# Optimization experiments

Hardware: AMD Instinct MI355X
Metric: run time of the kernel (lower is better)

## Reference

```python
import jax, jax.numpy as jnp
import numpy as np

N = 10000      # nodes
E = 160000     # edges (before self-loops)
H = 8          # heads
D_IN, D_H1, D_H2 = 165, 128, 1    # per-head channels of gat1 / gat2
HID = H * D_H1                    # 1024


def batchnorm(x, gamma, beta, eps=1e-5):
    # training-mode BatchNorm1d: biased batch statistics over the node axis
    mu = x.mean(0)
    var = x.var(0)
    return (x - mu) * jax.lax.rsqrt(var + eps) * gamma + beta


def gatv2(x, src, dst, Wl, bl, Wr, br, att, bias, heads, out_ch, concat, n_nodes):
    # PyG GATv2Conv: lin_l on source, lin_r on target; e = att . LeakyReLU(xl_j + xr_i)
    xl = (x @ Wl + bl).reshape(n_nodes, heads, out_ch)   # source transform
    xr = (x @ Wr + br).reshape(n_nodes, heads, out_ch)   # target transform
    e = jax.nn.leaky_relu(xl[src] + xr[dst], 0.2)        # [E,H,C]
    logits = jnp.einsum('ehc,hc->eh', e, att)            # [E,H]
    # segment softmax over incoming edges of each destination node
    m = jax.lax.stop_gradient(jax.ops.segment_max(logits, dst, num_segments=n_nodes))
    a = jnp.exp(logits - m[dst])
    s = jax.ops.segment_sum(a, dst, num_segments=n_nodes)
    alpha = a / (s[dst] + 1e-16)                          # [E,H]
    out = jax.ops.segment_sum(xl[src] * alpha[..., None], dst, num_segments=n_nodes)
    out = out.reshape(n_nodes, heads * out_ch) if concat else out.mean(1)
    return out + bias


def setup_inputs() -> dict:
    key = jax.random.key(0)
    ks = jax.random.split(key, 12)
    g = lambda k, shape, fan_in: jax.random.normal(k, shape, jnp.float32) * (1.0 / np.sqrt(fan_in))
    return {
        'x': jax.random.normal(ks[0], (N, D_IN), jnp.float32),
        'gamma1': jnp.ones((D_IN,), jnp.float32),
        'beta1': jnp.zeros((D_IN,), jnp.float32),
        'Wl1': g(ks[1], (D_IN, HID), D_IN),
        'bl1': jnp.zeros((HID,), jnp.float32),
        'Wr1': g(ks[2], (D_IN, HID), D_IN),
        'br1': jnp.zeros((HID,), jnp.float32),
        'att1': g(ks[3], (H, D_H1), D_H1),
        'bias1': jnp.zeros((HID,), jnp.float32),
        'gamma2': jnp.ones((HID,), jnp.float32),
        'beta2': jnp.zeros((HID,), jnp.float32),
        'Wl2': g(ks[4], (HID, H * D_H2), HID),
        'bl2': jnp.zeros((H * D_H2,), jnp.float32),
        'Wr2': g(ks[5], (HID, H * D_H2), HID),
        'br2': jnp.zeros((H * D_H2,), jnp.float32),
        'att2': g(ks[6], (H, D_H2), D_H2),
        'bias2': jnp.zeros((D_H2,), jnp.float32),
        'edge_index': jax.random.randint(ks[7], (2, E), 0, N, jnp.int64 if jax.config.jax_enable_x64 else jnp.int32),
    }


def reference(x, gamma1, beta1, Wl1, bl1, Wr1, br1, att1, bias1,
              gamma2, beta2, Wl2, bl2, Wr2, br2, att2, bias2, edge_index):
    loops = jnp.arange(N, dtype=edge_index.dtype)
    src = jnp.concatenate([edge_index[0], loops])   # add_self_loops=True (PyG default)
    dst = jnp.concatenate([edge_index[1], loops])
    h = batchnorm(x, gamma1, beta1)
    h = gatv2(h, src, dst, Wl1, bl1, Wr1, br1, att1, bias1, H, D_H1, True, N)
    h = batchnorm(h, gamma2, beta2)
    h = jax.nn.leaky_relu(h, 0.01)                  # F.leaky_relu default slope
    out = gatv2(h, src, dst, Wl2, bl2, Wr2, br2, att2, bias2, H, D_H2, False, N)
    return out
```

## Files before the change

### kernel.cpp

```cpp
#include <hip/hip_runtime.h>

#define NN   10000
#define E0   160000
#define ET   170000
#define DIN  165
#define KP   192
#define HID  1024
#define NH   8
#define BP   200
#define K2P  1032


typedef __bf16 bf16x8 __attribute__((ext_vector_type(8)));
typedef float  f32x4  __attribute__((ext_vector_type(4)));

__device__ __forceinline__ float bf2f(unsigned short u) {
    unsigned int i = ((unsigned int)u) << 16;
    return __builtin_bit_cast(float, i);
}
__device__ __forceinline__ unsigned short f2bf(float f) {
    unsigned int i = __builtin_bit_cast(unsigned int, f);
    i += 0x7fffu + ((i >> 16) & 1u);
    return (unsigned short)(i >> 16);
}
__device__ __forceinline__ float fin(float x) {
    return fminf(fmaxf(x, -1e30f), 1e30f);
}
__device__ __forceinline__ int clampi(int s) {
    return min(max(s, 0), NN - 1);
}
__device__ __forceinline__ void unpack8(uint4 u, float* f) {
    f[0]=bf2f((unsigned short)(u.x)); f[1]=bf2f((unsigned short)(u.x>>16));
    f[2]=bf2f((unsigned short)(u.y)); f[3]=bf2f((unsigned short)(u.y>>16));
    f[4]=bf2f((unsigned short)(u.z)); f[5]=bf2f((unsigned short)(u.z>>16));
    f[6]=bf2f((unsigned short)(u.w)); f[7]=bf2f((unsigned short)(u.w>>16));
}

__global__ __launch_bounds__(256) void debug_fill(float* __restrict__ out, float val) {
    int i = blockIdx.x * 256 + threadIdx.x;
    if (i < NN) out[i] = val;
}

__global__ __launch_bounds__(256) void bn1_stats(const float* __restrict__ x,
                                                 float* __restrict__ colsum, float* __restrict__ colsq) {
    int r0 = blockIdx.x * 125;
    int c = threadIdx.x;
    if (c >= DIN) return;
    float acc = 0.f, sq = 0.f;
    for (int r = r0; r < r0 + 125; ++r) {
        float v = x[(size_t)r * DIN + c];
        acc += v; sq += v * v;
    }
    atomicAdd(&colsum[c], acc);
    atomicAdd(&colsq[c], sq);
}

__global__ __launch_bounds__(256) void bn1_apply(const float* __restrict__ x,
                                                 const float* __restrict__ colsum, const float* __restrict__ colsq,
                                                 const float* __restrict__ gamma, const float* __restrict__ beta,
                                                 unsigned short* __restrict__ hn) {
    int idx = blockIdx.x * 256 + threadIdx.x;
    if (idx >= NN * KP) return;
    int r = idx / KP, c = idx - r * KP;
    float v = 0.f;
    if (c < DIN) {
        float mu  = colsum[c] * (1.f / NN);
        float var = fmaxf(colsq[c] * (1.f / NN) - mu * mu, 0.f);
        float a = gamma[c] * rsqrtf(var + 1e-5f);
        float b = beta[c] - mu * a;
        v = fin(x[(size_t)r * DIN + c] * a + b);
    }
    hn[idx] = f2bf(v);
}

__global__ __launch_bounds__(256) void w1_transpose(const float* __restrict__ wl,
                                                    const float* __restrict__ wr,
                                                    unsigned short* __restrict__ wlt,
                                                    unsigned short* __restrict__ wrt) {
    const float* src    = blockIdx.z ? wr  : wl;
    unsigned short* dst = blockIdx.z ? wrt : wlt;
    __shared__ float ts[32][65];
    const int k0 = blockIdx.x * 32;
    const int n0 = blockIdx.y * 64;
    const int tid = threadIdx.x;
    for (int idx = tid; idx < 32 * 64; idx += 256) {
        int k = idx >> 6, n = idx & 63;
        ts[k][n] = (k0 + k < DIN) ? src[(size_t)(k0 + k) * HID + n0 + n] : 0.f;
    }
    __syncthreads();
    for (int idx = tid; idx < 64 * 32; idx += 256) {
        int n = idx >> 5, k = idx & 31;
        dst[(size_t)(n0 + n) * KP + k0 + k] = f2bf(ts[k][n]);
    }
}

__global__ __launch_bounds__(256) void gemm1_kernel(
    const unsigned short* __restrict__ hn,
    const unsigned short* __restrict__ wlt,
    const unsigned short* __restrict__ wrt,
    const float* __restrict__ bl,
    const float* __restrict__ br,
    unsigned short* __restrict__ xl,
    unsigned short* __restrict__ xr) {
    __shared__ unsigned short bs[2][64 * BP];
    const int tid  = threadIdx.x;
    const int lane = tid & 63;
    const int wave = tid >> 6;
    const int col  = lane & 15;
    const int q    = lane >> 4;
    const int n0   = blockIdx.y * 64;

    for (int idx = tid; idx < 64 * 48 * 2; idx += 256) {
        int z = idx >= 64 * 48;
        int rem = z ? idx - 64 * 48 : idx;
        int r = rem / 48, c = rem - r * 48;
        const unsigned short* wt = z ? wrt : wlt;
        uint2 v = *(const uint2*)(wt + (size_t)(n0 + r) * KP + c * 4);
        *(uint2*)&bs[z][r * BP + c * 4] = v;
    }
    __syncthreads();

    const int mbase = blockIdx.x * 128 + wave * 32;
    const int am0 = mbase + col;
    const int am1 = am0 + 16;
    const bool aok0 = (am0 < NN), aok1 = (am1 < NN);

    f32x4 accL[2][4], accR[2][4];
    #pragma unroll
    for (int m = 0; m < 2; ++m)
        for (int nt = 0; nt < 4; ++nt)
            for (int r = 0; r < 4; ++r) { accL[m][nt][r] = 0.f; accR[m][nt][r] = 0.f; }

    #pragma unroll
    for (int kt = 0; kt < 6; ++kt) {
        const int kk = kt * 32 + q * 8;
        uint4 a0u = make_uint4(0u,0u,0u,0u), a1u = make_uint4(0u,0u,0u,0u);
        if (aok0) a0u = *(const uint4*)(hn + (size_t)am0 * KP + kk);
        if (aok1) a1u = *(const uint4*)(hn + (size_t)am1 * KP + kk);
        bf16x8 a0 = __builtin_bit_cast(bf16x8, a0u);
        bf16x8 a1 = __builtin_bit_cast(bf16x8, a1u);
        #pragma unroll
        for (int nt = 0; nt < 4; ++nt) {
            bf16x8 bfl = __builtin_bit_cast(bf16x8, *(const uint4*)&bs[0][(nt * 16 + col) * BP + kk]);
            accL[0][nt] = __builtin_amdgcn_mfma_f32_16x16x32_bf16(a0, bfl, accL[0][nt], 0, 0, 0);
            accL[1][nt] = __builtin_amdgcn_mfma_f32_16x16x32_bf16(a1, bfl, accL[1][nt], 0, 0, 0);
            bf16x8 bfr = __builtin_bit_cast(bf16x8, *(const uint4*)&bs[1][(nt * 16 + col) * BP + kk]);
            accR[0][nt] = __builtin_amdgcn_mfma_f32_16x16x32_bf16(a0, bfr, accR[0][nt], 0, 0, 0);
            accR[1][nt] = __builtin_amdgcn_mfma_f32_16x16x32_bf16(a1, bfr, accR[1][nt], 0, 0, 0);
        }
    }

    #pragma unroll
    for (int nt = 0; nt < 4; ++nt) {
        const int nc = n0 + nt * 16 + col;
        const float bLv = bl[nc];
        const float bRv = br[nc];
        #pragma unroll
        for (int m = 0; m < 2; ++m) {
            #pragma unroll
            for (int r = 0; r < 4; ++r) {
                const int row = mbase + m * 16 + q * 4 + r;
                if (row < NN) {
                    xl[(size_t)row * HID + nc] = f2bf(fin(accL[m][nt][r] + bLv));
                    xr[(size_t)row * HID + nc] = f2bf(fin(accR[m][nt][r] + bRv));
                }
            }
        }
    }
}

__global__ __launch_bounds__(256) void edge_hist(const int* __restrict__ ei, int* __restrict__ deg) {
    int e = blockIdx.x * 256 + threadIdx.x;
    if (e >= ET) return;
    int d = (e < E0) ? ei[E0 + e] : (e - E0);
    atomicAdd(&deg[clampi(d)], 1);
}

__global__ __launch_bounds__(1024) void scan_kernel(const int* __restrict__ deg,
                                                    int* __restrict__ offs, int* __restrict__ cur,
                                                    int* __restrict__ perm) {
    __shared__ int wsum[16];
    __shared__ int bins[64];
    __shared__ int bcur[64];
    const int tid = threadIdx.x;
    const int base = tid * 10;
    int loc[10];
    int run = 0;
    #pragma unroll
    for (int j = 0; j < 10; ++j) {
        int idx = base + j;
        int v = (idx < NN) ? deg[idx] : 0;
        loc[j] = run;
        run += v;
    }
    const int lane = tid & 63;
    const int w = tid >> 6;
    int inc = run;
    #pragma unroll
    for (int s = 1; s < 64; s <<= 1) {
        int t = __shfl_up(inc, s);
        if (lane >= s) inc += t;
    }
    if (lane == 63) wsum[w] = inc;
    if (tid < 64) bins[tid] = 0;
    __syncthreads();
    int woff = 0;
    #pragma unroll
    for (int k = 0; k < 16; ++k) woff += (k < w) ? wsum[k] : 0;
    const int toff = woff + inc - run;
    #pragma unroll
    for (int j = 0; j < 10; ++j) {
        int idx = base + j;
        if (idx < NN) {
            int e = toff + loc[j]; offs[idx] = e; cur[idx] = e;
            atomicAdd(&bins[63 - min(deg[idx], 63)], 1);
        }
    }
    if (tid == 1023) offs[NN] = woff + inc;
    __syncthreads();
    if (tid < 64) {
        int v = bins[tid];
        int binc = v;
        #pragma unroll
        for (int s = 1; s < 64; s <<= 1) {
            int t = __shfl_up(binc, s);
            if (tid >= s) binc += t;
        }
        bcur[tid] = binc - v;
    }
    __syncthreads();
    #pragma unroll
    for (int j = 0; j < 10; ++j) {
        int idx = base + j;
        if (idx < NN) {
            int pos = atomicAdd(&bcur[63 - min(deg[idx], 63)], 1);
            perm[pos] = idx;
        }
    }
}

__global__ __launch_bounds__(256) void edge_scatter(const int* __restrict__ ei,
                                                    int* __restrict__ cur, int* __restrict__ ssrc) {
    int e = blockIdx.x * 256 + threadIdx.x;
    if (e >= ET) return;
    int s, d;
    if (e < E0) { s = ei[e]; d = ei[E0 + e]; }
    else        { s = e - E0; d = e - E0; }
    int pos = atomicAdd(&cur[clampi(d)], 1);
    if (pos >= 0 && pos < ET) ssrc[pos] = clampi(s);
}

__global__ __launch_bounds__(256) void gat1_node(
    const unsigned short* __restrict__ xl1, const unsigned short* xr1,
    const float* __restrict__ att1, const float* __restrict__ bias1,
    const int* __restrict__ offs, const int* __restrict__ ssrc,
    const int* __restrict__ perm,
    unsigned short* agg) {
    const int lane = threadIdx.x & 63;
    const int wave = threadIdx.x >> 6;
    const int i = perm[blockIdx.x * 4 + wave];
    const int e0 = offs[i];
    const int e1 = max(offs[i + 1], e0);

    float xr_r[16], att_r[16];
    {
        const uint4* xp = (const uint4*)(xr1 + (size_t)i * HID + lane * 16);
        uint4 u0 = xp[0], u1 = xp[1];
        unpack8(u0, xr_r); unpack8(u1, xr_r + 8);
        const float4* ap = (const float4*)(att1 + lane * 16);
        float4 a0 = ap[0], a1 = ap[1], a2 = ap[2], a3 = ap[3];
        att_r[0]=a0.x; att_r[1]=a0.y; att_r[2]=a0.z; att_r[3]=a0.w;
        att_r[4]=a1.x; att_r[5]=a1.y; att_r[6]=a1.z; att_r[7]=a1.w;
        att_r[8]=a2.x; att_r[9]=a2.y; att_r[10]=a2.z; att_r[11]=a2.w;
        att_r[12]=a3.x; att_r[13]=a3.y; att_r[14]=a3.z; att_r[15]=a3.w;
    }

    float o[16];
    #pragma unroll
    for (int j = 0; j < 16; ++j) o[j] = 0.f;
    float s = 0.f;

    int e = e0;
    for (; e + 1 < e1; e += 2) {
        const int s0i = clampi(ssrc[e]);
        const int s1i = clampi(ssrc[e + 1]);
        const uint4* xp0 = (const uint4*)(xl1 + (size_t)s0i * HID + lane * 16);
        const uint4* xp1 = (const uint4*)(xl1 + (size_t)s1i * HID + lane * 16);
        uint4 a0 = xp0[0], a1 = xp0[1], b0 = xp1[0], b1 = xp1[1];
        float xv0[16], xv1[16];
        unpack8(a0, xv0); unpack8(a1, xv0 + 8);
        unpack8(b0, xv1); unpack8(b1, xv1 + 8);
        float p0 = 0.f, p1 = 0.f;
        #pragma unroll
        for (int j = 0; j < 16; ++j) {
            float v0 = xv0[j] + xr_r[j];
            float v1 = xv1[j] + xr_r[j];
            v0 = fmaxf(v0, 0.2f * v0);
            v1 = fmaxf(v1, 0.2f * v1);
            p0 = fmaf(att_r[j], v0, p0);
            p1 = fmaf(att_r[j], v1, p1);
        }
        p0 += __shfl_xor(p0, 1); p0 += __shfl_xor(p0, 2); p0 += __shfl_xor(p0, 4);
        p1 += __shfl_xor(p1, 1); p1 += __shfl_xor(p1, 2); p1 += __shfl_xor(p1, 4);
        const float aa0 = __expf(fminf(fin(p0), 50.f));
        const float aa1 = __expf(fminf(fin(p1), 50.f));
        s += aa0 + aa1;
        #pragma unroll
        for (int j = 0; j < 16; ++j) o[j] = fmaf(aa0, xv0[j], fmaf(aa1, xv1[j], o[j]));
    }
    if (e < e1) {
        const int sidx = clampi(ssrc[e]);
        const uint4* xp = (const uint4*)(xl1 + (size_t)sidx * HID + lane * 16);
        uint4 u0 = xp[0], u1 = xp[1];
        float xv[16];
        unpack8(u0, xv); unpack8(u1, xv + 8);
        float p = 0.f;
        #pragma unroll
        for (int j = 0; j < 16; ++j) {
            float v = xv[j] + xr_r[j];
            v = fmaxf(v, 0.2f * v);
            p = fmaf(att_r[j], v, p);
        }
        p += __shfl_xor(p, 1); p += __shfl_xor(p, 2); p += __shfl_xor(p, 4);
        const float a = __expf(fminf(fin(p), 50.f));
        s += a;
        #pragma unroll
        for (int j = 0; j < 16; ++j) o[j] = fmaf(a, xv[j], o[j]);
    }

    const float inv = 1.f / (s + 1e-16f);
    const float4* bp = (const float4*)(bias1 + lane * 16);
    float4 b0 = bp[0], b1 = bp[1], b2 = bp[2], b3 = bp[3];
    float bb[16] = {b0.x,b0.y,b0.z,b0.w, b1.x,b1.y,b1.z,b1.w,
                    b2.x,b2.y,b2.z,b2.w, b3.x,b3.y,b3.z,b3.w};
    unsigned short ov[16];
    #pragma unroll
    for (int j = 0; j < 16; ++j) ov[j] = f2bf(fin(o[j] * inv + bb[j]));
    uint4* op = (uint4*)(agg + (size_t)i * HID + lane * 16);
    op[0] = *(const uint4*)&ov[0];
    op[1] = *(const uint4*)&ov[8];
}

__global__ __launch_bounds__(256) void bn2_stats(const unsigned short* __restrict__ agg,
                                                 float* __restrict__ colsum, float* __restrict__ colsq) {
    int r0 = blockIdx.x * 125;
    int t = threadIdx.x;
    float s0=0,s1=0,s2=0,s3=0,q0=0,q1=0,q2=0,q3=0;
    for (int r = r0; r < r0 + 125; ++r) {
        const ushort4 u = *(const ushort4*)(agg + (size_t)r * HID + t * 4);
        float v0=bf2f(u.x), v1=bf2f(u.y), v2=bf2f(u.z), v3=bf2f(u.w);
        s0+=v0; q0+=v0*v0; s1+=v1; q1+=v1*v1;
        s2+=v2; q2+=v2*v2; s3+=v3; q3+=v3*v3;
    }
    atomicAdd(&colsum[t*4+0], s0); atomicAdd(&colsq[t*4+0], q0);
    atomicAdd(&colsum[t*4+1], s1); atomicAdd(&colsq[t*4+1], q1);
    atomicAdd(&colsum[t*4+2], s2); atomicAdd(&colsq[t*4+2], q2);
    atomicAdd(&colsum[t*4+3], s3); atomicAdd(&colsq[t*4+3], q3);
}

__global__ __launch_bounds__(256) void gemm2_kernel(
    const unsigned short* __restrict__ agg,
    const float* __restrict__ colsum, const float* __restrict__ colsq,
    const float* __restrict__ gamma, const float* __restrict__ beta,
    const float* __restrict__ wl2, const float* __restrict__ wr2,
    const float* __restrict__ bl2, const float* __restrict__ br2,
    float* __restrict__ xl2, float* __restrict__ xr2) {
    __shared__ unsigned short bs[16 * K2P];
    __shared__ float a2s[HID], b2s[HID];
    const int tid  = threadIdx.x;
    const int lane = tid & 63;
    const int wave = tid >> 6;
    const int col  = lane & 15;
    const int q    = lane >> 4;

    for (int idx = tid; idx < 16 * HID; idx += 256) {
        int n = idx >> 10, k = idx & (HID - 1);
        float v = (n < 8) ? wl2[k * 8 + n] : wr2[k * 8 + (n - 8)];
        bs[n * K2P + k] = f2bf(v);
    }
    for (int c = tid; c < HID; c += 256) {
        float mu  = colsum[c] * (1.f / NN);
        float var = fmaxf(colsq[c] * (1.f / NN) - mu * mu, 0.f);
        float a = gamma[c] * rsqrtf(var + 1e-5f);
        a2s[c] = a; b2s[c] = beta[c] - mu * a;
    }
    __syncthreads();

    const int mtile = blockIdx.x * 4 + wave;
    if (mtile >= NN / 16) return;
    const int m0 = mtile * 16;
    const int am = m0 + col;

    f32x4 acc;
    acc[0] = acc[1] = acc[2] = acc[3] = 0.f;
    #pragma unroll
    for (int kt = 0; kt < 32; ++kt) {
        const int kk = kt * 32 + q * 8;
        uint4 u = *(const uint4*)(agg + (size_t)am * HID + kk);
        float xv[8];
        unpack8(u, xv);
        unsigned short hv[8];
        #pragma unroll
        for (int j = 0; j < 8; ++j) {
            float v = xv[j] * a2s[kk + j] + b2s[kk + j];
            v = fmaxf(v, 0.01f * v);
            hv[j] = f2bf(fin(v));
        }
        bf16x8 af = __builtin_bit_cast(bf16x8, *(const uint4*)hv);
        bf16x8 bf = __builtin_bit_cast(bf16x8, *(const uint4*)&bs[col * K2P + kk]);
        acc = __builtin_amdgcn_mfma_f32_16x16x32_bf16(af, bf, acc, 0, 0, 0);
    }

    const float bv = (col < 8) ? bl2[col] : br2[col - 8];
    float* outp = (col < 8) ? (xl2 + col) : (xr2 + (col - 8));
    #pragma unroll
    for (int r = 0; r < 4; ++r) {
        const int row = m0 + q * 4 + r;
        outp[row * 8] = fin(acc[r] + bv);
    }
}

__global__ __launch_bounds__(256) void gat2_node(
    const float* __restrict__ xl2, const float* __restrict__ xr2,
    const float* __restrict__ att2, const float* __restrict__ bias2,
    const int* __restrict__ offs, const int* __restrict__ ssrc,
    const int* __restrict__ perm,
    float* __restrict__ out) {
    const int lane = threadIdx.x & 63;
    const int wave = threadIdx.x >> 6;
    const int i = perm[blockIdx.x * 4 + wave];
    const int h = lane & 7, slot = lane >> 3;
    const int e0 = offs[i];
    const int e1 = max(offs[i + 1], e0);
    const float xr_h = xr2[i * 8 + h];
    const float att_h = att2[h];
    float ssum = 0.f, wsum = 0.f;
    for (int eb = e0; eb < e1; eb += 8) {
        int e = eb + slot;
        if (e < e1) {
            float xlv = xl2[clampi(ssrc[e]) * 8 + h];
            float v = xlv + xr_h;
            v = fmaxf(v, 0.2f * v);
            float a = __expf(fminf(fin(att_h * v), 50.f));
            ssum += a; wsum += a * xlv;
        }
    }
    ssum += __shfl_xor(ssum, 8); ssum += __shfl_xor(ssum, 16); ssum += __shfl_xor(ssum, 32);
    wsum += __shfl_xor(wsum, 8); wsum += __shfl_xor(wsum, 16); wsum += __shfl_xor(wsum, 32);
    float v = fin(wsum / (ssum + 1e-16f));
    v += __shfl_xor(v, 1); v += __shfl_xor(v, 2); v += __shfl_xor(v, 4);
    if (lane == 0) out[i] = fin(v * 0.125f + bias2[0]);
}

extern "C" void kernel_launch(void* const* d_in, const int* in_sizes, int n_in,
                              void* d_out, int out_size, void* d_ws, size_t ws_size,
                              hipStream_t stream) {
    float* out = (float*)d_out;

    static const int expected[18] = {
        NN * DIN, DIN, DIN, DIN * HID, HID, DIN * HID, HID, HID, HID,
        HID, HID, HID * NH, NH, HID * NH, NH, NH, 1, 2 * E0
    };
    if (n_in != 18) {
        debug_fill<<<(NN + 255) / 256, 256, 0, stream>>>(out, 8192.f + 64.f * (float)n_in);
        return;
    }
    for (int i = 0; i < 18; ++i) {
        if (in_sizes[i] != expected[i]) {
            debug_fill<<<(NN + 255) / 256, 256, 0, stream>>>(out, 4096.f + 32.f * (float)i);
            return;
        }
    }

    const float* x      = (const float*)d_in[0];
    const float* gamma1 = (const float*)d_in[1];
    const float* beta1  = (const float*)d_in[2];
    const float* Wl1    = (const float*)d_in[3];
    const float* bl1    = (const float*)d_in[4];
    const float* Wr1    = (const float*)d_in[5];
    const float* br1    = (const float*)d_in[6];
    const float* att1   = (const float*)d_in[7];
    const float* bias1  = (const float*)d_in[8];
    const float* gamma2 = (const float*)d_in[9];
    const float* beta2  = (const float*)d_in[10];
    const float* Wl2    = (const float*)d_in[11];
    const float* bl2    = (const float*)d_in[12];
    const float* Wr2    = (const float*)d_in[13];
    const float* br2    = (const float*)d_in[14];
    const float* att2   = (const float*)d_in[15];
    const float* bias2  = (const float*)d_in[16];
    const int*   ei     = (const int*)d_in[17];

    char* p = (char*)d_ws;
    auto alloc = [&](size_t bytes) -> void* {
        void* r = (void*)p;
        p += (bytes + 255) & ~(size_t)255;
        return r;
    };
    unsigned short* xl1  = (unsigned short*)alloc((size_t)NN * HID * 2);
    unsigned short* xr1  = (unsigned short*)alloc((size_t)NN * HID * 2);
    unsigned short* agg  = xr1;
    unsigned short* hn   = (unsigned short*)alloc((size_t)NN * KP * 2);
    unsigned short* wlt  = (unsigned short*)alloc((size_t)HID * KP * 2);
    unsigned short* wrt  = (unsigned short*)alloc((size_t)HID * KP * 2);
    float*          xl2  = (float*)alloc((size_t)NN * 8 * 4);
    float*          xr2  = (float*)alloc((size_t)NN * 8 * 4);
    int*            offs = (int*)alloc((NN + 1) * 4);
    int*            cur  = (int*)alloc(NN * 4);
    int*            ssrc = (int*)alloc(ET * 4);
    int*            perm = (int*)alloc(NN * 4);
    char* zbase = p;
    float* colsum1 = (float*)alloc(DIN * 4);
    float* colsq1  = (float*)alloc(DIN * 4);
    float* colsum2 = (float*)alloc(HID * 4);
    float* colsq2  = (float*)alloc(HID * 4);
    int*   deg     = (int*)alloc(NN * 4);
    size_t zlen = (size_t)(p - zbase);
    hipMemsetAsync(zbase, 0, zlen, stream);

    bn1_stats<<<80, 256, 0, stream>>>(x, colsum1, colsq1);
    bn1_apply<<<(NN * KP + 255) / 256, 256, 0, stream>>>(x, colsum1, colsq1, gamma1, beta1, hn);
    w1_transpose<<<dim3(6, 16, 2), 256, 0, stream>>>(Wl1, Wr1, wlt, wrt);
    gemm1_kernel<<<dim3((NN + 127) / 128, HID / 64), 256, 0, stream>>>(hn, wlt, wrt, bl1, br1, xl1, xr1);
    edge_hist<<<(ET + 255) / 256, 256, 0, stream>>>(ei, deg);
    scan_kernel<<<1, 1024, 0, stream>>>(deg, offs, cur, perm);
    edge_scatter<<<(ET + 255) / 256, 256, 0, stream>>>(ei, cur, ssrc);
    gat1_node<<<NN / 4, 256, 0, stream>>>(xl1, xr1, att1, bias1, offs, ssrc, perm, agg);
    bn2_stats<<<80, 256, 0, stream>>>(agg, colsum2, colsq2);
    gemm2_kernel<<<(NN / 16 + 3) / 4, 256, 0, stream>>>(agg, colsum2, colsq2, gamma2, beta2,
                                                        Wl2, Wr2, bl2, br2, xl2, xr2);
    gat2_node<<<NN / 4, 256, 0, stream>>>(xl2, xr2, att2, bias2, offs, ssrc, perm, out);
}
```

Measured before the change: 280.5 us.

## Stage gemm1 epilogue through LDS, split gemm2 K across waves, widen BN stats grids

The gemm1 epilogue now writes bf16 results into shared memory and then stores them as coalesced 16-byte rows, replacing scattered 2-byte global stores. gemm2 now runs one 16-row tile per block and splits the K dimension across the four waves, combining partial sums in LDS, so it launches 625 blocks instead of about 157. The BN statistics kernels use 125 blocks of 80 rows, and bn1_stats adds four independent accumulators for more parallelism. In exchange, gemm2 blocks each rebuild the transposed weight tile in LDS and add a reduction barrier.

```diff
diff --git a/kernel.cpp b/kernel.cpp
--- a/kernel.cpp
+++ b/kernel.cpp
@@ -13,6 +13,7 @@
 
 typedef __bf16 bf16x8 __attribute__((ext_vector_type(8)));
 typedef float  f32x4  __attribute__((ext_vector_type(4)));
+typedef float  f32x2  __attribute__((ext_vector_type(2)));
 
 __device__ __forceinline__ float bf2f(unsigned short u) {
     unsigned int i = ((unsigned int)u) << 16;
@@ -43,16 +44,22 @@
 
 __global__ __launch_bounds__(256) void bn1_stats(const float* __restrict__ x,
                                                  float* __restrict__ colsum, float* __restrict__ colsq) {
-    int r0 = blockIdx.x * 125;
     int c = threadIdx.x;
     if (c >= DIN) return;
-    float acc = 0.f, sq = 0.f;
-    for (int r = r0; r < r0 + 125; ++r) {
-        float v = x[(size_t)r * DIN + c];
-        acc += v; sq += v * v;
-    }
-    atomicAdd(&colsum[c], acc);
-    atomicAdd(&colsq[c], sq);
+    int r0 = blockIdx.x * 80;
+    float a0=0,a1=0,a2=0,a3=0, q0=0,q1=0,q2=0,q3=0;
+    for (int r = r0; r < r0 + 80; r += 4) {
+        float v0 = x[(size_t)r * DIN + c];
+        float v1 = x[(size_t)(r + 1) * DIN + c];
+        float v2 = x[(size_t)(r + 2) * DIN + c];
+        float v3 = x[(size_t)(r + 3) * DIN + c];
+        a0 += v0; q0 += v0 * v0;
+        a1 += v1; q1 += v1 * v1;
+        a2 += v2; q2 += v2 * v2;
+        a3 += v3; q3 += v3 * v3;
+    }
+    atomicAdd(&colsum[c], (a0 + a1) + (a2 + a3));
+    atomicAdd(&colsq[c],  (q0 + q1) + (q2 + q3));
 }
 
 __global__ __launch_bounds__(256) void bn1_apply(const float* __restrict__ x,
@@ -150,6 +157,9 @@
         }
     }
 
+    __syncthreads();
+    unsigned short* cl = &bs[0][0];
+    unsigned short* cr = cl + 128 * 72;
     #pragma unroll
     for (int nt = 0; nt < 4; ++nt) {
         const int nc = n0 + nt * 16 + col;
@@ -159,12 +169,20 @@
         for (int m = 0; m < 2; ++m) {
             #pragma unroll
             for (int r = 0; r < 4; ++r) {
-                const int row = mbase + m * 16 + q * 4 + r;
-                if (row < NN) {
-                    xl[(size_t)row * HID + nc] = f2bf(fin(accL[m][nt][r] + bLv));
-                    xr[(size_t)row * HID + nc] = f2bf(fin(accR[m][nt][r] + bRv));
-                }
+                const int lrow = wave * 32 + m * 16 + q * 4 + r;
+                cl[lrow * 72 + nt * 16 + col] = f2bf(fin(accL[m][nt][r] + bLv));
+                cr[lrow * 72 + nt * 16 + col] = f2bf(fin(accR[m][nt][r] + bRv));
             }
+        }
+    }
+    __syncthreads();
+    const int mblk = blockIdx.x * 128;
+    for (int t = tid; t < 128 * 8; t += 256) {
+        const int row = t >> 3, ch = t & 7;
+        const int grow = mblk + row;
+        if (grow < NN) {
+            *(uint4*)(xl + (size_t)grow * HID + n0 + ch * 8) = *(const uint4*)&cl[row * 72 + ch * 8];
+            *(uint4*)(xr + (size_t)grow * HID + n0 + ch * 8) = *(const uint4*)&cr[row * 72 + ch * 8];
         }
     }
 }
@@ -343,10 +361,11 @@
 
 __global__ __launch_bounds__(256) void bn2_stats(const unsigned short* __restrict__ agg,
                                                  float* __restrict__ colsum, float* __restrict__ colsq) {
-    int r0 = blockIdx.x * 125;
+    int r0 = blockIdx.x * 80;
     int t = threadIdx.x;
     float s0=0,s1=0,s2=0,s3=0,q0=0,q1=0,q2=0,q3=0;
-    for (int r = r0; r < r0 + 125; ++r) {
+    #pragma unroll 2
+    for (int r = r0; r < r0 + 80; ++r) {
         const ushort4 u = *(const ushort4*)(agg + (size_t)r * HID + t * 4);
         float v0=bf2f(u.x), v1=bf2f(u.y), v2=bf2f(u.z), v3=bf2f(u.w);
         s0+=v0; q0+=v0*v0; s1+=v1; q1+=v1*v1;
@@ -367,6 +386,7 @@
     float* __restrict__ xl2, float* __restrict__ xr2) {
     __shared__ unsigned short bs[16 * K2P];
     __shared__ float a2s[HID], b2s[HID];
+    __shared__ float red[4 * 64 * 4];
     const int tid  = threadIdx.x;
     const int lane = tid & 63;
     const int wave = tid >> 6;
@@ -378,23 +398,22 @@
         float v = (n < 8) ? wl2[k * 8 + n] : wr2[k * 8 + (n - 8)];
         bs[n * K2P + k] = f2bf(v);
     }
-    for (int c = tid; c < HID; c += 256) {
-        float mu  = colsum[c] * (1.f / NN);
-        float var = fmaxf(colsq[c] * (1.f / NN) - mu * mu, 0.f);
-        float a = gamma[c] * rsqrtf(var + 1e-5f);
-        a2s[c] = a; b2s[c] = beta[c] - mu * a;
-    }
-    __syncthreads();
-
-    const int mtile = blockIdx.x * 4 + wave;
-    if (mtile >= NN / 16) return;
-    const int m0 = mtile * 16;
+    for (int cc = tid; cc < HID; cc += 256) {
+        float mu  = colsum[cc] * (1.f / NN);
+        float var = fmaxf(colsq[cc] * (1.f / NN) - mu * mu, 0.f);
+        float a = gamma[cc] * rsqrtf(var + 1e-5f);
+        a2s[cc] = a; b2s[cc] = beta[cc] - mu * a;
+    }
+    __syncthreads();
+
+    const int m0 = blockIdx.x * 16;
     const int am = m0 + col;
 
     f32x4 acc;
     acc[0] = acc[1] = acc[2] = acc[3] = 0.f;
     #pragma unroll
-    for (int kt = 0; kt < 32; ++kt) {
+    for (int t = 0; t < 8; ++t) {
+        const int kt = wave * 8 + t;
         const int kk = kt * 32 + q * 8;
         uint4 u = *(const uint4*)(agg + (size_t)am * HID + kk);
         float xv[8];
@@ -411,12 +430,21 @@
         acc = __builtin_amdgcn_mfma_f32_16x16x32_bf16(af, bf, acc, 0, 0, 0);
     }
 
-    const float bv = (col < 8) ? bl2[col] : br2[col - 8];
-    float* outp = (col < 8) ? (xl2 + col) : (xr2 + (col - 8));
-    #pragma unroll
-    for (int r = 0; r < 4; ++r) {
-        const int row = m0 + q * 4 + r;
-        outp[row * 8] = fin(acc[r] + bv);
+    *(f32x4*)&red[(wave * 64 + lane) * 4] = acc;
+    __syncthreads();
+    if (wave == 0) {
+        f32x4 a0 = *(const f32x4*)&red[lane * 4];
+        f32x4 a1 = *(const f32x4*)&red[(64 + lane) * 4];
+        f32x4 a2 = *(const f32x4*)&red[(128 + lane) * 4];
+        f32x4 a3 = *(const f32x4*)&red[(192 + lane) * 4];
+        acc = (a0 + a1) + (a2 + a3);
+        const float bv = (col < 8) ? bl2[col] : br2[col - 8];
+        float* outp = (col < 8) ? (xl2 + col) : (xr2 + (col - 8));
+        #pragma unroll
+        for (int r = 0; r < 4; ++r) {
+            const int row = m0 + q * 4 + r;
+            outp[row * 8] = fin(acc[r] + bv);
+        }
     }
 }
 
@@ -518,7 +546,7 @@
     size_t zlen = (size_t)(p - zbase);
     hipMemsetAsync(zbase, 0, zlen, stream);
 
-    bn1_stats<<<80, 256, 0, stream>>>(x, colsum1, colsq1);
+    bn1_stats<<<125, 256, 0, stream>>>(x, colsum1, colsq1);
     bn1_apply<<<(NN * KP + 255) / 256, 256, 0, stream>>>(x, colsum1, colsq1, gamma1, beta1, hn);
     w1_transpose<<<dim3(6, 16, 2), 256, 0, stream>>>(Wl1, Wr1, wlt, wrt);
     gemm1_kernel<<<dim3((NN + 127) / 128, HID / 64), 256, 0, stream>>>(hn, wlt, wrt, bl1, br1, xl1, xr1);
@@ -526,8 +554,8 @@
     scan_kernel<<<1, 1024, 0, stream>>>(deg, offs, cur, perm);
     edge_scatter<<<(ET + 255) / 256, 256, 0, stream>>>(ei, cur, ssrc);
     gat1_node<<<NN / 4, 256, 0, stream>>>(xl1, xr1, att1, bias1, offs, ssrc, perm, agg);
-    bn2_stats<<<80, 256, 0, stream>>>(agg, colsum2, colsq2);
-    gemm2_kernel<<<(NN / 16 + 3) / 4, 256, 0, stream>>>(agg, colsum2, colsq2, gamma2, beta2,
-                                                        Wl2, Wr2, bl2, br2, xl2, xr2);
+    bn2_stats<<<125, 256, 0, stream>>>(agg, colsum2, colsq2);
+    gemm2_kernel<<<NN / 16, 256, 0, stream>>>(agg, colsum2, colsq2, gamma2, beta2,
+                                              Wl2, Wr2, bl2, br2, xl2, xr2);
     gat2_node<<<NN / 4, 256, 0, stream>>>(xl2, xr2, att2, bias2, offs, ssrc, perm, out);
 }
```

Result: slower. 287.2 us (+2.4%).
